# Kernel tuning notes

Hardware: AMD Instinct MI355X
Metric: run time of the kernel (lower is better)

The kernel has to match this reference:

```python
import jax, jax.numpy as jnp
import numpy as np

B, N, C = 2, 1024, 61          # images, proposals/img, classes (incl. background)
W, H = 1024.0, 1024.0          # image size
K = 100                        # detections_per_img
SCORE_THRESH = 0.05
NMS_THRESH = 0.5
WX, WY, WW, WH = 10.0, 10.0, 5.0, 5.0        # Box2BoxTransform weights
SCALE_CLAMP = float(np.log(1000.0 / 16.0))


def decode(deltas, boxes):
    # deltas [N, C*4], boxes [N, 4] xyxy -> [N, C, 4] xyxy
    widths = boxes[:, 2] - boxes[:, 0]
    heights = boxes[:, 3] - boxes[:, 1]
    ctr_x = boxes[:, 0] + 0.5 * widths
    ctr_y = boxes[:, 1] + 0.5 * heights
    d = deltas.reshape(boxes.shape[0], -1, 4)
    dx, dy = d[..., 0] / WX, d[..., 1] / WY
    dw = jnp.minimum(d[..., 2] / WW, SCALE_CLAMP)
    dh = jnp.minimum(d[..., 3] / WH, SCALE_CLAMP)
    pcx = dx * widths[:, None] + ctr_x[:, None]
    pcy = dy * heights[:, None] + ctr_y[:, None]
    pw = jnp.exp(dw) * widths[:, None]
    ph = jnp.exp(dh) * heights[:, None]
    return jnp.stack([pcx - 0.5 * pw, pcy - 0.5 * ph,
                      pcx + 0.5 * pw, pcy + 0.5 * ph], axis=-1)


def iou_matrix(b):
    # b [N, 4] xyxy -> pairwise IoU [N, N]
    area = (b[:, 2] - b[:, 0]) * (b[:, 3] - b[:, 1])
    lt = jnp.maximum(b[:, None, :2], b[None, :, :2])
    rb = jnp.minimum(b[:, None, 2:], b[None, :, 2:])
    wh = jnp.clip(rb - lt, 0.0)
    inter = wh[..., 0] * wh[..., 1]
    return inter / (area[:, None] + area[None, :] - inter + 1e-9)


def nms_keep(iou, valid):
    # greedy NMS over score-sorted boxes; iou [N,N], valid [N] -> keep [N]
    def body(sup, i):
        keep_i = valid[i] & jnp.logical_not(sup[i])
        sup = sup | (keep_i & (iou[i] > NMS_THRESH))
        return sup, keep_i
    _, keep = jax.lax.scan(body, jnp.zeros(valid.shape[0], bool),
                           jnp.arange(valid.shape[0]))
    return keep


def per_class(boxes_j, scores_j):
    # boxes_j [N,4], scores_j [N]: threshold, sort desc, NMS
    valid = scores_j > SCORE_THRESH
    key_s = jnp.where(valid, scores_j, -1.0)
    order = jnp.argsort(-key_s)
    b, v, s = boxes_j[order], valid[order], key_s[order]
    keep = nms_keep(iou_matrix(b), v)
    return jnp.where(keep[:, None], b, 0.0), jnp.where(keep, s, 0.0)


def per_image(logits, deltas, props):
    probs = jax.nn.softmax(logits, axis=-1)           # [N, C]
    boxes = decode(deltas, props)                     # [N, C, 4]
    boxes = jnp.stack([jnp.clip(boxes[..., 0], 0.0, W),
                       jnp.clip(boxes[..., 1], 0.0, H),
                       jnp.clip(boxes[..., 2], 0.0, W),
                       jnp.clip(boxes[..., 3], 0.0, H)], axis=-1)
    boxes_fg = jnp.transpose(boxes[:, 1:, :], (1, 0, 2))   # [C-1, N, 4]
    scores_fg = probs[:, 1:].T                              # [C-1, N]
    b_k, s_k = jax.vmap(per_class)(boxes_fg, scores_fg)
    labels = jnp.broadcast_to(jnp.arange(1, C, dtype=jnp.int32)[:, None], (C - 1, N))
    s_flat = s_k.reshape(-1)
    b_flat = b_k.reshape(-1, 4)
    l_flat = labels.reshape(-1)
    top_s, top_i = jax.lax.top_k(s_flat, K)
    dets = jnp.concatenate([b_flat[top_i], top_s[:, None]], axis=-1)  # [K, 5]
    return dets, l_flat[top_i]


def setup_inputs() -> dict:
    key = jax.random.key(0)
    k1, k2, k3, k4 = jax.random.split(key, 4)
    class_logits = jax.random.normal(k1, (B * N, C), dtype=jnp.float32) * 2.0
    box_regression = jax.random.normal(k2, (B * N, C * 4), dtype=jnp.float32) * 0.5
    cxcy = jax.random.uniform(k3, (B, N, 2), dtype=jnp.float32) * jnp.array([W, H], jnp.float32)
    wh = jax.random.uniform(k4, (B, N, 2), dtype=jnp.float32) * 160.0 + 16.0
    proposals = jnp.concatenate([jnp.clip(cxcy - 0.5 * wh, 0.0),
                                 jnp.minimum(cxcy + 0.5 * wh,
                                             jnp.array([W, H], jnp.float32))], axis=-1)
    return {"class_logits": class_logits, "box_regression": box_regression,
            "proposals": proposals}


def reference(class_logits, box_regression, proposals):
    logits = class_logits.reshape(B, N, C)
    deltas = box_regression.reshape(B, N, C * 4)
    dets, labels = jax.vmap(per_image)(logits, deltas, proposals)
    return dets, labels  # [B, K, 5] (xyxy+score), [B, K] int32 labels
```

## Files before the change

### kernel.cpp

```cpp
#include <hip/hip_runtime.h>
#include <math.h>

#define NB   2
#define NP   1024
#define NC   61
#define NFG  60
#define KTOP 100
#define CAP  61440
#define SELCAP 2048

__device__ __forceinline__ float clampf(float x, float lo, float hi) {
  return fminf(fmaxf(x, lo), hi);
}

__global__ void rowstats_kernel(const float* __restrict__ logits,
                                float* __restrict__ rowmax,
                                float* __restrict__ rowsum,
                                int* __restrict__ ccnt) {
  if (blockIdx.x == 0 && threadIdx.x < NB) ccnt[threadIdx.x] = 0;
  int wave = threadIdx.x >> 6, lane = threadIdx.x & 63;
  int row = blockIdx.x * 4 + wave;
  if (row >= NB * NP) return;
  float x = (lane < NC) ? logits[row * NC + lane] : -INFINITY;
  float m = x;
  #pragma unroll
  for (int o = 32; o; o >>= 1) m = fmaxf(m, __shfl_xor(m, o, 64));
  float e = (lane < NC) ? expf(x - m) : 0.0f;
  float s = e;
  #pragma unroll
  for (int o = 32; o; o >>= 1) s += __shfl_xor(s, o, 64);
  if (lane == 0) { rowmax[row] = m; rowsum[row] = s; }
}

__global__ void __launch_bounds__(64)
nms_kernel(const float* __restrict__ logits,
           const float* __restrict__ deltas,
           const float* __restrict__ props,
           const float* __restrict__ rowmax,
           const float* __restrict__ rowsum,
           float* __restrict__ cscore,
           int* __restrict__ cflat,
           int* __restrict__ clabel,
           float* __restrict__ cbox,
           int* __restrict__ ccnt) {
  const float SCALE_CLAMP = 4.135166556742356f;
  int b = blockIdx.x / NFG;
  int j = blockIdx.x % NFG;
  int cls = j + 1;
  int lane = threadIdx.x;
  unsigned long long lt = (1ull << lane) - 1ull;

  __shared__ unsigned long long ukey[NP];
  __shared__ unsigned long long skey[NP];
  __shared__ float sbox[NP][4];

  int nv = 0;
  #pragma unroll 4
  for (int c = 0; c < NP / 64; ++c) {
    int n = c * 64 + lane;
    int row = b * NP + n;
    float sc = expf(logits[row * NC + cls] - rowmax[row]) / rowsum[row];
    bool pred = sc > 0.05f;
    unsigned long long m = __ballot(pred);
    if (pred) {
      int pos = nv + __popcll(m & lt);
      ukey[pos] = ((unsigned long long)__float_as_uint(sc) << 32)
                | (unsigned)(NP - 1 - n);
    }
    nv += __popcll(m);
  }
  __syncthreads();
  if (nv == 0) return;
  int chunks = (nv + 63) >> 6;

  for (int c = 0; c < chunks; ++c) {
    int e = c * 64 + lane;
    if (e < nv) {
      unsigned long long ke = ukey[e];
      int r = 0;
      for (int m2 = 0; m2 < nv; ++m2) r += (ukey[m2] > ke) ? 1 : 0;
      skey[r] = ke;
    }
  }
  __syncthreads();

  for (int c = 0; c < chunks; ++c) {
    int p = c * 64 + lane;
    if (p < nv) {
      unsigned long long k = skey[p];
      int n = NP - 1 - (int)(k & 0xFFFFull);
      int row = b * NP + n;
      const float* pr = props + row * 4;
      float w = pr[2] - pr[0], h = pr[3] - pr[1];
      float cx = pr[0] + 0.5f * w, cy = pr[1] + 0.5f * h;
      const float* dd = deltas + (size_t)row * (NC * 4) + cls * 4;
      float dx = dd[0] / 10.0f, dy = dd[1] / 10.0f;
      float dw = fminf(dd[2] / 5.0f, SCALE_CLAMP);
      float dh = fminf(dd[3] / 5.0f, SCALE_CLAMP);
      float pcx = dx * w + cx, pcy = dy * h + cy;
      float pw = expf(dw) * w, ph = expf(dh) * h;
      sbox[p][0] = clampf(pcx - 0.5f * pw, 0.0f, 1024.0f);
      sbox[p][1] = clampf(pcy - 0.5f * ph, 0.0f, 1024.0f);
      sbox[p][2] = clampf(pcx + 0.5f * pw, 0.0f, 1024.0f);
      sbox[p][3] = clampf(pcy + 0.5f * ph, 0.0f, 1024.0f);
    }
  }
  __syncthreads();

  unsigned int supbits = 0, keptbits = 0;
  for (int i = 0; i < nv; ++i) {
    int ci = i >> 6, bi = i & 63;
    unsigned long long supmask = __ballot((supbits >> ci) & 1u);
    if ((supmask >> bi) & 1ull) continue;
    keptbits |= ((lane == bi) ? 1u : 0u) << ci;
    float bx1 = sbox[i][0], by1 = sbox[i][1];
    float bx2 = sbox[i][2], by2 = sbox[i][3];
    float ai = (bx2 - bx1) * (by2 - by1);
    for (int c = 0; c < chunks; ++c) {
      int p = c * 64 + lane;
      float t1 = sbox[p][0], t2 = sbox[p][1];
      float t3 = sbox[p][2], t4 = sbox[p][3];
      float at = (t3 - t1) * (t4 - t2);
      float iw = fmaxf(fminf(bx2, t3) - fmaxf(bx1, t1), 0.0f);
      float ih = fmaxf(fminf(by2, t4) - fmaxf(by1, t2), 0.0f);
      float inter = iw * ih;
      float iou = inter / (ai + at - inter + 1e-9f);
      bool s = (p < nv) && (iou > 0.5f);
      supbits |= (s ? 1u : 0u) << c;
    }
  }

  int total = 0;
  for (int c = 0; c < chunks; ++c)
    total += __popcll(__ballot((keptbits >> c) & 1u));
  int base = 0;
  if (lane == 0) base = atomicAdd(&ccnt[b], total);
  base = __shfl(base, 0);
  int prior = 0;
  for (int c = 0; c < chunks; ++c) {
    unsigned long long mask = __ballot((keptbits >> c) & 1u);
    if ((keptbits >> c) & 1u) {
      int slot = base + prior + __popcll(mask & lt);
      int p = c * 64 + lane;
      int g = b * CAP + slot;
      cscore[g] = __uint_as_float((unsigned)(skey[p] >> 32));
      cflat[g]  = j * NP + p;
      clabel[g] = cls;
      cbox[g * 4 + 0] = sbox[p][0];
      cbox[g * 4 + 1] = sbox[p][1];
      cbox[g * 4 + 2] = sbox[p][2];
      cbox[g * 4 + 3] = sbox[p][3];
    }
    prior += __popcll(mask);
  }
}

__global__ void __launch_bounds__(256)
topk_kernel(const float* __restrict__ cscore,
            const int* __restrict__ cflat,
            const int* __restrict__ clabel,
            const float* __restrict__ cbox,
            const int* __restrict__ ccnt,
            float* __restrict__ out) {
  int b = blockIdx.x;
  int tid = threadIdx.x;
  int cnt = ccnt[b]; if (cnt > CAP) cnt = CAP;
  const float* cs = cscore + b * CAP;
  const int* cf = cflat + b * CAP;

  __shared__ int hist[256];
  __shared__ int s_thr, s_sel;
  __shared__ float sel_s[SELCAP];
  __shared__ int sel_f[SELCAP];
  __shared__ int sel_i[SELCAP];
  __shared__ int order[KTOP];

  for (int i = tid; i < 256; i += 256) hist[i] = 0;
  __syncthreads();
  for (int i = tid; i < cnt; i += 256) {
    float s = cs[i];
    int bin = (int)(s * 256.0f);
    bin = bin < 0 ? 0 : (bin > 255 ? 255 : bin);
    atomicAdd(&hist[bin], 1);
  }
  __syncthreads();
  if (tid == 0) {
    int acc = 0, t = 255;
    for (; t >= 0; --t) { acc += hist[t]; if (acc >= KTOP) break; }
    s_thr = (acc >= KTOP) ? t : 0;
    s_sel = 0;
  }
  __syncthreads();
  int thr = s_thr;
  for (int i = tid; i < cnt; i += 256) {
    float s = cs[i];
    int bin = (int)(s * 256.0f);
    bin = bin < 0 ? 0 : (bin > 255 ? 255 : bin);
    if (bin >= thr) {
      int p = atomicAdd(&s_sel, 1);
      if (p < SELCAP) { sel_s[p] = s; sel_f[p] = cf[i]; sel_i[p] = i; }
    }
  }
  __syncthreads();
  int nsel = s_sel < SELCAP ? s_sel : SELCAP;

  for (int e = tid; e < nsel; e += 256) {
    float ke = sel_s[e]; int fe = sel_f[e];
    int r = 0;
    for (int m = 0; m < nsel; ++m) {
      float km = sel_s[m]; int fm = sel_f[m];
      if (km > ke || (km == ke && fm < fe)) ++r;
    }
    if (r < KTOP) order[r] = e;
  }
  __syncthreads();

  for (int k = tid; k < KTOP; k += 256) {
    float* det = out + (size_t)(b * KTOP + k) * 5;
    float lab;
    if (k < nsel) {
      int e = order[k];
      int ci = sel_i[e];
      const float* bxp = cbox + (size_t)(b * CAP + ci) * 4;
      det[0] = bxp[0]; det[1] = bxp[1]; det[2] = bxp[2]; det[3] = bxp[3];
      det[4] = sel_s[e];
      lab = (float)clabel[b * CAP + ci];
    } else {
      det[0] = det[1] = det[2] = det[3] = 0.0f;
      det[4] = 0.0f;
      lab = 1.0f;
    }
    out[NB * KTOP * 5 + b * KTOP + k] = lab;
  }
}

extern "C" void kernel_launch(void* const* d_in, const int* in_sizes, int n_in,
                              void* d_out, int out_size, void* d_ws, size_t ws_size,
                              hipStream_t stream) {
  (void)in_sizes; (void)n_in; (void)out_size; (void)ws_size;
  const float* logits = (const float*)d_in[0];
  const float* deltas = (const float*)d_in[1];
  const float* props  = (const float*)d_in[2];
  float* out = (float*)d_out;

  float* wf     = (float*)d_ws;
  float* rowmax = wf;
  float* rowsum = wf + NB * NP;
  int*   ccnt   = (int*)(wf + 2 * NB * NP);
  float* cscore = wf + 2 * NB * NP + 4;
  int*   cflat  = (int*)(cscore + (size_t)NB * CAP);
  int*   clabel = (int*)(cscore + 2 * (size_t)NB * CAP);
  float* cbox   = cscore + 3 * (size_t)NB * CAP;

  rowstats_kernel<<<(NB * NP) / 4, 256, 0, stream>>>(logits, rowmax, rowsum, ccnt);
  nms_kernel<<<NB * NFG, 64, 0, stream>>>(logits, deltas, props, rowmax, rowsum,
                                          cscore, cflat, clabel, cbox, ccnt);
  topk_kernel<<<NB, 256, 0, stream>>>(cscore, cflat, clabel, cbox, ccnt, out);
}
```

Baseline: 123.1 us.

## Fuse softmax, per-class NMS and top-k into one cooperative kernel

Replaces the three kernel launches with one cooperative kernel that uses grid syncs between the softmax, per-class NMS and top-k stages. Softmax scores are written transposed per class so the NMS blocks read them coalesced. For classes with at most 256 candidates, the boxes stay in registers and a precomputed IoU bitmask (built with ballots) drives the greedy pass. Top-k uses a wave-level scan and writes output straight from a rank sort. This removes launch overhead and redundant per-element softmax recomputation, at the cost of grid-sync latency, only a single wave per block in top-k, and a reduced CAP that clips candidates if there are too many.

New measurement: 201.3 us. 63.6% more time.

```diff
diff --git a/kernel.cpp b/kernel.cpp
--- a/kernel.cpp
+++ b/kernel.cpp
@@ -1,236 +1,343 @@
 #include <hip/hip_runtime.h>
+#include <hip/hip_cooperative_groups.h>
 #include <math.h>
+
+namespace cg = cooperative_groups;
 
 #define NB   2
 #define NP   1024
 #define NC   61
 #define NFG  60
 #define KTOP 100
-#define CAP  61440
-#define SELCAP 2048
+#define CAP  20480
+#define MAXSEL 4096
+#define GRID (NB*NFG)
+
+typedef unsigned long long u64;
 
 __device__ __forceinline__ float clampf(float x, float lo, float hi) {
   return fminf(fmaxf(x, lo), hi);
 }
 
-__global__ void rowstats_kernel(const float* __restrict__ logits,
-                                float* __restrict__ rowmax,
-                                float* __restrict__ rowsum,
-                                int* __restrict__ ccnt) {
-  if (blockIdx.x == 0 && threadIdx.x < NB) ccnt[threadIdx.x] = 0;
-  int wave = threadIdx.x >> 6, lane = threadIdx.x & 63;
-  int row = blockIdx.x * 4 + wave;
-  if (row >= NB * NP) return;
-  float x = (lane < NC) ? logits[row * NC + lane] : -INFINITY;
-  float m = x;
-  #pragma unroll
-  for (int o = 32; o; o >>= 1) m = fmaxf(m, __shfl_xor(m, o, 64));
-  float e = (lane < NC) ? expf(x - m) : 0.0f;
-  float s = e;
-  #pragma unroll
-  for (int o = 32; o; o >>= 1) s += __shfl_xor(s, o, 64);
-  if (lane == 0) { rowmax[row] = m; rowsum[row] = s; }
-}
-
 __global__ void __launch_bounds__(64)
-nms_kernel(const float* __restrict__ logits,
-           const float* __restrict__ deltas,
-           const float* __restrict__ props,
-           const float* __restrict__ rowmax,
-           const float* __restrict__ rowsum,
-           float* __restrict__ cscore,
-           int* __restrict__ cflat,
-           int* __restrict__ clabel,
-           float* __restrict__ cbox,
-           int* __restrict__ ccnt) {
+fused_kernel(const float* __restrict__ logits,
+             const float* __restrict__ deltas,
+             const float* __restrict__ props,
+             float* __restrict__ scores_t,
+             float* __restrict__ cscore,
+             int* __restrict__ cflat,
+             int* __restrict__ clabel,
+             float* __restrict__ cbox,
+             int* __restrict__ ccnt,
+             float* __restrict__ out) {
   const float SCALE_CLAMP = 4.135166556742356f;
-  int b = blockIdx.x / NFG;
-  int j = blockIdx.x % NFG;
-  int cls = j + 1;
   int lane = threadIdx.x;
-  unsigned long long lt = (1ull << lane) - 1ull;
-
-  __shared__ unsigned long long ukey[NP];
-  __shared__ unsigned long long skey[NP];
-  __shared__ float sbox[NP][4];
-
-  int nv = 0;
-  #pragma unroll 4
-  for (int c = 0; c < NP / 64; ++c) {
-    int n = c * 64 + lane;
-    int row = b * NP + n;
-    float sc = expf(logits[row * NC + cls] - rowmax[row]) / rowsum[row];
-    bool pred = sc > 0.05f;
-    unsigned long long m = __ballot(pred);
-    if (pred) {
-      int pos = nv + __popcll(m & lt);
-      ukey[pos] = ((unsigned long long)__float_as_uint(sc) << 32)
-                | (unsigned)(NP - 1 - n);
-    }
-    nv += __popcll(m);
+  u64 lt = (1ull << lane) - 1ull;
+
+  __shared__ __align__(16) unsigned char smem[50176];
+  u64* ukey = (u64*)smem;
+  u64* skey = (u64*)(smem + 8192);
+  float (*sbox)[4] = (float(*)[4])(smem + 16384);
+
+  cg::grid_group grid = cg::this_grid();
+
+  if (blockIdx.x == 0 && lane < NB) ccnt[lane] = 0;
+  for (int row = blockIdx.x; row < NB * NP; row += GRID) {
+    float x = (lane < NC) ? logits[(size_t)row * NC + lane] : -INFINITY;
+    float m = x;
+    #pragma unroll
+    for (int o = 32; o; o >>= 1) m = fmaxf(m, __shfl_xor(m, o, 64));
+    float e = (lane < NC) ? expf(x - m) : 0.0f;
+    float s = e;
+    #pragma unroll
+    for (int o = 32; o; o >>= 1) s += __shfl_xor(s, o, 64);
+    if (lane >= 1 && lane < NC)
+      scores_t[(size_t)((row >> 10) * NFG + (lane - 1)) * NP + (row & (NP - 1))] = e / s;
   }
-  __syncthreads();
-  if (nv == 0) return;
-  int chunks = (nv + 63) >> 6;
-
-  for (int c = 0; c < chunks; ++c) {
-    int e = c * 64 + lane;
-    if (e < nv) {
-      unsigned long long ke = ukey[e];
+  grid.sync();
+
+  int b = blockIdx.x / NFG, j = blockIdx.x % NFG, cls = j + 1;
+  {
+    const float* scol = scores_t + (size_t)(b * NFG + j) * NP;
+    float sc[16];
+    #pragma unroll
+    for (int c = 0; c < 16; ++c) sc[c] = scol[c * 64 + lane];
+    int nv = 0;
+    #pragma unroll
+    for (int c = 0; c < 16; ++c) {
+      bool pred = sc[c] > 0.05f;
+      u64 m = __ballot(pred);
+      if (pred)
+        ukey[nv + __popcll(m & lt)] =
+            ((u64)__float_as_uint(sc[c]) << 32) | (unsigned)(NP - 1 - (c * 64 + lane));
+      nv += (int)__popcll(m);
+    }
+    __syncthreads();
+    int chunks = (nv + 63) >> 6;
+
+    for (int c = 0; c < chunks; ++c) {
+      int e = c * 64 + lane;
+      if (e < nv) {
+        u64 ke = ukey[e];
+        int r = 0;
+        for (int m2 = 0; m2 < nv; ++m2) r += (ukey[m2] > ke) ? 1 : 0;
+        skey[r] = ke;
+      }
+    }
+    __syncthreads();
+
+    if (nv > 0 && nv <= 256) {
+      float x0[4], y0[4], x1[4], y1[4], ar[4], scr[4];
+      #pragma unroll
+      for (int c = 0; c < 4; ++c) {
+        x0[c] = y0[c] = x1[c] = y1[c] = 1e30f; ar[c] = 0.0f; scr[c] = 0.0f;
+        int p = c * 64 + lane;
+        if (c < chunks && p < nv) {
+          u64 k = skey[p];
+          scr[c] = __uint_as_float((unsigned)(k >> 32));
+          int n = NP - 1 - (int)(k & 0xFFFFull);
+          int row = b * NP + n;
+          float4 pr = *(const float4*)(props + (size_t)row * 4);
+          float w = pr.z - pr.x, h = pr.w - pr.y;
+          float cx = pr.x + 0.5f * w, cy = pr.y + 0.5f * h;
+          float4 dd = *(const float4*)(deltas + (size_t)row * (NC * 4) + cls * 4);
+          float dx = dd.x / 10.0f, dy = dd.y / 10.0f;
+          float dw = fminf(dd.z / 5.0f, SCALE_CLAMP);
+          float dh = fminf(dd.w / 5.0f, SCALE_CLAMP);
+          float pcx = dx * w + cx, pcy = dy * h + cy;
+          float pw = expf(dw) * w, ph = expf(dh) * h;
+          x0[c] = clampf(pcx - 0.5f * pw, 0.0f, 1024.0f);
+          y0[c] = clampf(pcy - 0.5f * ph, 0.0f, 1024.0f);
+          x1[c] = clampf(pcx + 0.5f * pw, 0.0f, 1024.0f);
+          y1[c] = clampf(pcy + 0.5f * ph, 0.0f, 1024.0f);
+          ar[c] = (x1[c] - x0[c]) * (y1[c] - y0[c]);
+        }
+      }
+
+      u64 rows_r[4][4];
+      #pragma unroll
+      for (int a = 0; a < 4; ++a)
+        #pragma unroll
+        for (int c2 = 0; c2 < 4; ++c2) rows_r[a][c2] = 0;
+
+      for (int i = 0; i < nv; ++i) {
+        int ci = i >> 6, bi = i & 63;
+        float t0 = x0[0], t1 = y0[0], t2 = x1[0], t3 = y1[0], ta = ar[0];
+        #pragma unroll
+        for (int c = 1; c < 4; ++c)
+          if (ci == c) { t0 = x0[c]; t1 = y0[c]; t2 = x1[c]; t3 = y1[c]; ta = ar[c]; }
+        float ix0 = __shfl(t0, bi), iy0 = __shfl(t1, bi);
+        float ix1 = __shfl(t2, bi), iy1 = __shfl(t3, bi);
+        float ia  = __shfl(ta, bi);
+        #pragma unroll
+        for (int c2 = 0; c2 < 4; ++c2) if (c2 < chunks) {
+          float iw = fmaxf(fminf(ix1, x1[c2]) - fmaxf(ix0, x0[c2]), 0.0f);
+          float ih = fmaxf(fminf(iy1, y1[c2]) - fmaxf(iy0, y0[c2]), 0.0f);
+          float inter = iw * ih;
+          float iou = inter / (ia + ar[c2] - inter + 1e-9f);
+          u64 mb = __ballot(iou > 0.5f);
+          #pragma unroll
+          for (int a = 0; a < 4; ++a)
+            if (a == ci && lane == bi) rows_r[a][c2] = mb;
+        }
+      }
+
+      u64 supm[4] = {0, 0, 0, 0}, keptm[4] = {0, 0, 0, 0};
+      for (int i = 0; i < nv; ++i) {
+        int ci = i >> 6, bi = i & 63;
+        u64 sv = supm[0];
+        #pragma unroll
+        for (int c = 1; c < 4; ++c) if (ci == c) sv = supm[c];
+        if ((sv >> bi) & 1ull) continue;
+        #pragma unroll
+        for (int c = 0; c < 4; ++c) if (ci == c) keptm[c] |= (1ull << bi);
+        #pragma unroll
+        for (int c2 = 0; c2 < 4; ++c2) if (c2 < chunks) {
+          u64 rr = rows_r[0][c2];
+          #pragma unroll
+          for (int c = 1; c < 4; ++c) if (ci == c) rr = rows_r[c][c2];
+          rr = __shfl(rr, bi);
+          supm[c2] |= rr;
+        }
+      }
+
+      int total = 0;
+      #pragma unroll
+      for (int c = 0; c < 4; ++c) total += (int)__popcll(keptm[c]);
+      int basei = 0;
+      if (lane == 0 && total > 0) basei = atomicAdd(&ccnt[b], total);
+      basei = __shfl(basei, 0);
+      int prior = 0;
+      #pragma unroll
+      for (int c = 0; c < 4; ++c) if (c < chunks) {
+        u64 mk = keptm[c];
+        if ((mk >> lane) & 1ull) {
+          int slot = basei + prior + (int)__popcll(mk & lt);
+          if (slot < CAP) {
+            int g = b * CAP + slot;
+            cscore[g] = scr[c];
+            cflat[g]  = j * NP + (c * 64 + lane);
+            clabel[g] = cls;
+            float4 bb; bb.x = x0[c]; bb.y = y0[c]; bb.z = x1[c]; bb.w = y1[c];
+            *(float4*)(cbox + (size_t)g * 4) = bb;
+          }
+        }
+        prior += (int)__popcll(mk);
+      }
+    } else if (nv > 256) {
+      for (int c = 0; c < chunks; ++c) {
+        int p = c * 64 + lane;
+        if (p < nv) {
+          u64 k = skey[p];
+          int n = NP - 1 - (int)(k & 0xFFFFull);
+          int row = b * NP + n;
+          float4 pr = *(const float4*)(props + (size_t)row * 4);
+          float w = pr.z - pr.x, h = pr.w - pr.y;
+          float cx = pr.x + 0.5f * w, cy = pr.y + 0.5f * h;
+          float4 dd = *(const float4*)(deltas + (size_t)row * (NC * 4) + cls * 4);
+          float dx = dd.x / 10.0f, dy = dd.y / 10.0f;
+          float dw = fminf(dd.z / 5.0f, SCALE_CLAMP);
+          float dh = fminf(dd.w / 5.0f, SCALE_CLAMP);
+          float pcx = dx * w + cx, pcy = dy * h + cy;
+          float pw = expf(dw) * w, ph = expf(dh) * h;
+          sbox[p][0] = clampf(pcx - 0.5f * pw, 0.0f, 1024.0f);
+          sbox[p][1] = clampf(pcy - 0.5f * ph, 0.0f, 1024.0f);
+          sbox[p][2] = clampf(pcx + 0.5f * pw, 0.0f, 1024.0f);
+          sbox[p][3] = clampf(pcy + 0.5f * ph, 0.0f, 1024.0f);
+        }
+      }
+      __syncthreads();
+      unsigned int supbits = 0, keptbits = 0;
+      for (int i = 0; i < nv; ++i) {
+        int ci = i >> 6, bi = i & 63;
+        u64 supmask = __ballot((supbits >> ci) & 1u);
+        if ((supmask >> bi) & 1ull) continue;
+        keptbits |= ((lane == bi) ? 1u : 0u) << ci;
+        float bx1 = sbox[i][0], by1 = sbox[i][1], bx2 = sbox[i][2], by2 = sbox[i][3];
+        float ai = (bx2 - bx1) * (by2 - by1);
+        for (int c = 0; c < chunks; ++c) {
+          int p = c * 64 + lane;
+          float t1 = sbox[p][0], t2 = sbox[p][1], t3 = sbox[p][2], t4 = sbox[p][3];
+          float at = (t3 - t1) * (t4 - t2);
+          float iw = fmaxf(fminf(bx2, t3) - fmaxf(bx1, t1), 0.0f);
+          float ih = fmaxf(fminf(by2, t4) - fmaxf(by1, t2), 0.0f);
+          float inter = iw * ih;
+          float iou = inter / (ai + at - inter + 1e-9f);
+          bool s = (p < nv) && (iou > 0.5f);
+          supbits |= (s ? 1u : 0u) << c;
+        }
+      }
+      int total = 0;
+      for (int c = 0; c < chunks; ++c)
+        total += (int)__popcll(__ballot((keptbits >> c) & 1u));
+      int basei = 0;
+      if (lane == 0 && total > 0) basei = atomicAdd(&ccnt[b], total);
+      basei = __shfl(basei, 0);
+      int prior = 0;
+      for (int c = 0; c < chunks; ++c) {
+        u64 mask = __ballot((keptbits >> c) & 1u);
+        if ((keptbits >> c) & 1u) {
+          int slot = basei + prior + (int)__popcll(mask & lt);
+          int p = c * 64 + lane;
+          if (slot < CAP) {
+            int g = b * CAP + slot;
+            cscore[g] = __uint_as_float((unsigned)(skey[p] >> 32));
+            cflat[g]  = j * NP + p;
+            clabel[g] = cls;
+            float4 bb; bb.x = sbox[p][0]; bb.y = sbox[p][1]; bb.z = sbox[p][2]; bb.w = sbox[p][3];
+            *(float4*)(cbox + (size_t)g * 4) = bb;
+          }
+        }
+        prior += (int)__popcll(mask);
+      }
+    }
+  }
+  grid.sync();
+
+  if (blockIdx.x < NB) {
+    int bb = blockIdx.x;
+    int cnt = ccnt[bb]; if (cnt > CAP) cnt = CAP;
+    const float* cs = cscore + (size_t)bb * CAP;
+    const int* cf = cflat + (size_t)bb * CAP;
+    int* hist = (int*)smem;
+    u64* sel_k = (u64*)(smem + 1024);
+    int* sel_i = (int*)(smem + 1024 + 8 * MAXSEL);
+
+    for (int i = lane; i < 256; i += 64) hist[i] = 0;
+    __syncthreads();
+    for (int i = lane; i < cnt; i += 64) {
+      int bin = (int)(cs[i] * 256.0f);
+      bin = bin < 0 ? 0 : (bin > 255 ? 255 : bin);
+      atomicAdd(&hist[bin], 1);
+    }
+    __syncthreads();
+
+    int c0 = hist[lane * 4 + 0], c1 = hist[lane * 4 + 1];
+    int c2 = hist[lane * 4 + 2], c3 = hist[lane * 4 + 3];
+    int sl = c0 + c1 + c2 + c3;
+    int suf = sl;
+    #pragma unroll
+    for (int off = 1; off < 64; off <<= 1) {
+      int idx = lane + off;
+      int v = __shfl(suf, idx < 64 ? idx : 63, 64);
+      suf += (idx < 64) ? v : 0;
+    }
+    int basec = suf - sl;
+    int f3 = basec + c3, f2 = f3 + c2, f1 = f2 + c1, f0 = f1 + c0;
+    int best = -1;
+    if (f3 >= KTOP) best = lane * 4 + 3;
+    else if (f2 >= KTOP) best = lane * 4 + 2;
+    else if (f1 >= KTOP) best = lane * 4 + 1;
+    else if (f0 >= KTOP) best = lane * 4 + 0;
+    #pragma unroll
+    for (int off = 32; off; off >>= 1) {
+      int o = __shfl_xor(best, off, 64);
+      best = best > o ? best : o;
+    }
+    int thr = best < 0 ? 0 : best;
+
+    int nsel = 0;
+    for (int i0 = 0; i0 < cnt; i0 += 64) {
+      int i = i0 + lane;
+      bool pred = false; u64 key = 0;
+      if (i < cnt) {
+        float s_ = cs[i];
+        int bin = (int)(s_ * 256.0f);
+        bin = bin < 0 ? 0 : (bin > 255 ? 255 : bin);
+        if (bin >= thr) {
+          pred = true;
+          key = ((u64)__float_as_uint(s_) << 32) | (unsigned)(65535 - cf[i]);
+        }
+      }
+      u64 m = __ballot(pred);
+      if (pred) {
+        int pos = nsel + (int)__popcll(m & lt);
+        if (pos < MAXSEL) { sel_k[pos] = key; sel_i[pos] = i; }
+      }
+      nsel += (int)__popcll(m);
+    }
+    if (nsel > MAXSEL) nsel = MAXSEL;
+    __syncthreads();
+
+    for (int e = lane; e < nsel; e += 64) {
+      u64 ke = sel_k[e];
       int r = 0;
-      for (int m2 = 0; m2 < nv; ++m2) r += (ukey[m2] > ke) ? 1 : 0;
-      skey[r] = ke;
-    }
-  }
-  __syncthreads();
-
-  for (int c = 0; c < chunks; ++c) {
-    int p = c * 64 + lane;
-    if (p < nv) {
-      unsigned long long k = skey[p];
-      int n = NP - 1 - (int)(k & 0xFFFFull);
-      int row = b * NP + n;
-      const float* pr = props + row * 4;
-      float w = pr[2] - pr[0], h = pr[3] - pr[1];
-      float cx = pr[0] + 0.5f * w, cy = pr[1] + 0.5f * h;
-      const float* dd = deltas + (size_t)row * (NC * 4) + cls * 4;
-      float dx = dd[0] / 10.0f, dy = dd[1] / 10.0f;
-      float dw = fminf(dd[2] / 5.0f, SCALE_CLAMP);
-      float dh = fminf(dd[3] / 5.0f, SCALE_CLAMP);
-      float pcx = dx * w + cx, pcy = dy * h + cy;
-      float pw = expf(dw) * w, ph = expf(dh) * h;
-      sbox[p][0] = clampf(pcx - 0.5f * pw, 0.0f, 1024.0f);
-      sbox[p][1] = clampf(pcy - 0.5f * ph, 0.0f, 1024.0f);
-      sbox[p][2] = clampf(pcx + 0.5f * pw, 0.0f, 1024.0f);
-      sbox[p][3] = clampf(pcy + 0.5f * ph, 0.0f, 1024.0f);
-    }
-  }
-  __syncthreads();
-
-  unsigned int supbits = 0, keptbits = 0;
-  for (int i = 0; i < nv; ++i) {
-    int ci = i >> 6, bi = i & 63;
-    unsigned long long supmask = __ballot((supbits >> ci) & 1u);
-    if ((supmask >> bi) & 1ull) continue;
-    keptbits |= ((lane == bi) ? 1u : 0u) << ci;
-    float bx1 = sbox[i][0], by1 = sbox[i][1];
-    float bx2 = sbox[i][2], by2 = sbox[i][3];
-    float ai = (bx2 - bx1) * (by2 - by1);
-    for (int c = 0; c < chunks; ++c) {
-      int p = c * 64 + lane;
-      float t1 = sbox[p][0], t2 = sbox[p][1];
-      float t3 = sbox[p][2], t4 = sbox[p][3];
-      float at = (t3 - t1) * (t4 - t2);
-      float iw = fmaxf(fminf(bx2, t3) - fmaxf(bx1, t1), 0.0f);
-      float ih = fmaxf(fminf(by2, t4) - fmaxf(by1, t2), 0.0f);
-      float inter = iw * ih;
-      float iou = inter / (ai + at - inter + 1e-9f);
-      bool s = (p < nv) && (iou > 0.5f);
-      supbits |= (s ? 1u : 0u) << c;
-    }
-  }
-
-  int total = 0;
-  for (int c = 0; c < chunks; ++c)
-    total += __popcll(__ballot((keptbits >> c) & 1u));
-  int base = 0;
-  if (lane == 0) base = atomicAdd(&ccnt[b], total);
-  base = __shfl(base, 0);
-  int prior = 0;
-  for (int c = 0; c < chunks; ++c) {
-    unsigned long long mask = __ballot((keptbits >> c) & 1u);
-    if ((keptbits >> c) & 1u) {
-      int slot = base + prior + __popcll(mask & lt);
-      int p = c * 64 + lane;
-      int g = b * CAP + slot;
-      cscore[g] = __uint_as_float((unsigned)(skey[p] >> 32));
-      cflat[g]  = j * NP + p;
-      clabel[g] = cls;
-      cbox[g * 4 + 0] = sbox[p][0];
-      cbox[g * 4 + 1] = sbox[p][1];
-      cbox[g * 4 + 2] = sbox[p][2];
-      cbox[g * 4 + 3] = sbox[p][3];
-    }
-    prior += __popcll(mask);
-  }
-}
-
-__global__ void __launch_bounds__(256)
-topk_kernel(const float* __restrict__ cscore,
-            const int* __restrict__ cflat,
-            const int* __restrict__ clabel,
-            const float* __restrict__ cbox,
-            const int* __restrict__ ccnt,
-            float* __restrict__ out) {
-  int b = blockIdx.x;
-  int tid = threadIdx.x;
-  int cnt = ccnt[b]; if (cnt > CAP) cnt = CAP;
-  const float* cs = cscore + b * CAP;
-  const int* cf = cflat + b * CAP;
-
-  __shared__ int hist[256];
-  __shared__ int s_thr, s_sel;
-  __shared__ float sel_s[SELCAP];
-  __shared__ int sel_f[SELCAP];
-  __shared__ int sel_i[SELCAP];
-  __shared__ int order[KTOP];
-
-  for (int i = tid; i < 256; i += 256) hist[i] = 0;
-  __syncthreads();
-  for (int i = tid; i < cnt; i += 256) {
-    float s = cs[i];
-    int bin = (int)(s * 256.0f);
-    bin = bin < 0 ? 0 : (bin > 255 ? 255 : bin);
-    atomicAdd(&hist[bin], 1);
-  }
-  __syncthreads();
-  if (tid == 0) {
-    int acc = 0, t = 255;
-    for (; t >= 0; --t) { acc += hist[t]; if (acc >= KTOP) break; }
-    s_thr = (acc >= KTOP) ? t : 0;
-    s_sel = 0;
-  }
-  __syncthreads();
-  int thr = s_thr;
-  for (int i = tid; i < cnt; i += 256) {
-    float s = cs[i];
-    int bin = (int)(s * 256.0f);
-    bin = bin < 0 ? 0 : (bin > 255 ? 255 : bin);
-    if (bin >= thr) {
-      int p = atomicAdd(&s_sel, 1);
-      if (p < SELCAP) { sel_s[p] = s; sel_f[p] = cf[i]; sel_i[p] = i; }
-    }
-  }
-  __syncthreads();
-  int nsel = s_sel < SELCAP ? s_sel : SELCAP;
-
-  for (int e = tid; e < nsel; e += 256) {
-    float ke = sel_s[e]; int fe = sel_f[e];
-    int r = 0;
-    for (int m = 0; m < nsel; ++m) {
-      float km = sel_s[m]; int fm = sel_f[m];
-      if (km > ke || (km == ke && fm < fe)) ++r;
-    }
-    if (r < KTOP) order[r] = e;
-  }
-  __syncthreads();
-
-  for (int k = tid; k < KTOP; k += 256) {
-    float* det = out + (size_t)(b * KTOP + k) * 5;
-    float lab;
-    if (k < nsel) {
-      int e = order[k];
-      int ci = sel_i[e];
-      const float* bxp = cbox + (size_t)(b * CAP + ci) * 4;
-      det[0] = bxp[0]; det[1] = bxp[1]; det[2] = bxp[2]; det[3] = bxp[3];
-      det[4] = sel_s[e];
-      lab = (float)clabel[b * CAP + ci];
-    } else {
+      for (int m2 = 0; m2 < nsel; ++m2) r += (sel_k[m2] > ke) ? 1 : 0;
+      if (r < KTOP) {
+        int ci = sel_i[e];
+        float4 bx = *(const float4*)(cbox + (size_t)(bb * CAP + ci) * 4);
+        float* det = out + (size_t)(bb * KTOP + r) * 5;
+        det[0] = bx.x; det[1] = bx.y; det[2] = bx.z; det[3] = bx.w;
+        det[4] = __uint_as_float((unsigned)(ke >> 32));
+        out[NB * KTOP * 5 + bb * KTOP + r] = (float)clabel[bb * CAP + ci];
+      }
+    }
+    for (int k = nsel + lane; k < KTOP; k += 64) {
+      float* det = out + (size_t)(bb * KTOP + k) * 5;
       det[0] = det[1] = det[2] = det[3] = 0.0f;
       det[4] = 0.0f;
-      lab = 1.0f;
-    }
-    out[NB * KTOP * 5 + b * KTOP + k] = lab;
+      out[NB * KTOP * 5 + bb * KTOP + k] = 1.0f;
+    }
   }
 }
 
@@ -243,17 +350,17 @@
   const float* props  = (const float*)d_in[2];
   float* out = (float*)d_out;
 
-  float* wf     = (float*)d_ws;
-  float* rowmax = wf;
-  float* rowsum = wf + NB * NP;
-  int*   ccnt   = (int*)(wf + 2 * NB * NP);
-  float* cscore = wf + 2 * NB * NP + 4;
-  int*   cflat  = (int*)(cscore + (size_t)NB * CAP);
-  int*   clabel = (int*)(cscore + 2 * (size_t)NB * CAP);
-  float* cbox   = cscore + 3 * (size_t)NB * CAP;
-
-  rowstats_kernel<<<(NB * NP) / 4, 256, 0, stream>>>(logits, rowmax, rowsum, ccnt);
-  nms_kernel<<<NB * NFG, 64, 0, stream>>>(logits, deltas, props, rowmax, rowsum,
-                                          cscore, cflat, clabel, cbox, ccnt);
-  topk_kernel<<<NB, 256, 0, stream>>>(cscore, cflat, clabel, cbox, ccnt, out);
+  float* wf       = (float*)d_ws;
+  float* scores_t = wf;
+  float* cscore   = wf + 122880;
+  float* cbox     = wf + 163840;
+  int*   cflat    = (int*)(wf + 327680);
+  int*   clabel   = (int*)(wf + 368640);
+  int*   ccnt     = (int*)(wf + 409600);
+
+  void* args[10] = {(void*)&logits, (void*)&deltas, (void*)&props,
+                    (void*)&scores_t, (void*)&cscore, (void*)&cflat,
+                    (void*)&clabel, (void*)&cbox, (void*)&ccnt, (void*)&out};
+  hipLaunchCooperativeKernel((const void*)fused_kernel, dim3(GRID), dim3(64),
+                             args, 0, stream);
 }
```
